# Performance work log

Measured on AMD Instinct MI355X. Metric: run time of the kernel, lower is better.

The kernel has to match this reference:

```python
import jax, jax.numpy as jnp
import numpy as np

B, T, C = 2, 2048, 1024
H = 16
D = C // H  # head_dim = 64
SCALE = D ** -0.5


def setup_inputs() -> dict:
    key = jax.random.key(0)
    ks = jax.random.split(key, 5)
    x = jax.random.normal(ks[0], (B, T, C), dtype=jnp.float32)
    # causal mask: -inf above diagonal, 0 elsewhere (module checks mask == -inf)
    neg_inf = jnp.float32(-jnp.inf)
    causal = jnp.where(jnp.tril(jnp.ones((T, T), dtype=bool)), 0.0, neg_inf)
    mask = causal[None, None, :, :].astype(jnp.float32)  # [1,1,T,T]
    # xavier_normal for [C, C] linear weights: std = sqrt(2/(C+C))
    std = float(np.sqrt(2.0 / (C + C)))
    wq = jax.random.normal(ks[1], (C, C), dtype=jnp.float32) * std
    wk = jax.random.normal(ks[2], (C, C), dtype=jnp.float32) * std
    wv = jax.random.normal(ks[3], (C, C), dtype=jnp.float32) * std
    wo = jax.random.normal(ks[4], (C, C), dtype=jnp.float32) * std
    return {"x": x, "mask": mask, "wq": wq, "wk": wk, "wv": wv, "wo": wo}


def reference(x, mask, wq, wk, wv, wo):
    # torch nn.Linear: y = x @ W.T
    q = jnp.einsum('btc,oc->bto', x, wq).reshape(B, T, H, D).transpose(0, 2, 1, 3)
    k = jnp.einsum('btc,oc->bto', x, wk).reshape(B, T, H, D).transpose(0, 2, 1, 3)
    v = jnp.einsum('btc,oc->bto', x, wv).reshape(B, T, H, D).transpose(0, 2, 1, 3)
    scores = jnp.einsum('bhqd,bhkd->bhqk', q, k) * SCALE  # [B,H,T,T]
    scores = jnp.where(mask == -jnp.inf, -jnp.inf, scores)
    attn = jax.nn.softmax(scores, axis=-1)
    out = jnp.einsum('bhqk,bhkd->bhqd', attn, v)  # [B,H,T,D]
    out = out.transpose(0, 2, 1, 3).reshape(B, T, C)
    return jnp.einsum('btc,oc->bto', out, wo)
```

## Files before the change

kernel.cpp:

```cpp
#include <hip/hip_runtime.h>
#include <hip/hip_bf16.h>


typedef __bf16 bf16_t;
typedef __bf16 bf16x8 __attribute__((ext_vector_type(8)));
typedef __bf16 bf16x4 __attribute__((ext_vector_type(4)));
typedef float  f32x4  __attribute__((ext_vector_type(4)));

__device__ __forceinline__ void gload_lds16(const bf16_t* g, bf16_t* l) {
  __builtin_amdgcn_global_load_lds((__attribute__((address_space(1))) void*)g,
                                   (__attribute__((address_space(3))) void*)l, 16, 0, 0);
}

__global__ __launch_bounds__(256) void cvt_f32_bf16(const float* __restrict__ in,
                                                    bf16_t* __restrict__ out, int n4) {
  int i = blockIdx.x * 256 + threadIdx.x;
  if (i >= n4) return;
  float4 v = reinterpret_cast<const float4*>(in)[i];
  bf16x4 o;
  o[0] = (bf16_t)v.x; o[1] = (bf16_t)v.y; o[2] = (bf16_t)v.z; o[3] = (bf16_t)v.w;
  reinterpret_cast<bf16x4*>(out)[i] = o;
}

__global__ __launch_bounds__(256) void cvt_w4(const float* __restrict__ i0, const float* __restrict__ i1,
                                              const float* __restrict__ i2, const float* __restrict__ i3,
                                              bf16_t* __restrict__ o0, bf16_t* __restrict__ o1,
                                              bf16_t* __restrict__ o2, bf16_t* __restrict__ o3) {
  int which = blockIdx.y;
  const float* in = (which == 0) ? i0 : (which == 1) ? i1 : (which == 2) ? i2 : i3;
  bf16_t* out     = (which == 0) ? o0 : (which == 1) ? o1 : (which == 2) ? o2 : o3;
  int i = blockIdx.x * 256 + threadIdx.x;
  float4 v = reinterpret_cast<const float4*>(in)[i];
  bf16x4 o;
  o[0] = (bf16_t)v.x; o[1] = (bf16_t)v.y; o[2] = (bf16_t)v.z; o[3] = (bf16_t)v.w;
  reinterpret_cast<bf16x4*>(out)[i] = o;
}

#define TM 128
#define TN 128
#define TK 64

__global__ __launch_bounds__(256) void gemm_bt(
    const bf16_t* __restrict__ A,
    const bf16_t* __restrict__ W0, const bf16_t* __restrict__ W1, const bf16_t* __restrict__ W2,
    bf16_t* __restrict__ O0, bf16_t* __restrict__ O1, bf16_t* __restrict__ O2,
    float* __restrict__ OF, int kind)
{
  __shared__ alignas(16) bf16_t As[TM * TK];
  __shared__ alignas(16) bf16_t Bs[TN * TK];
  const int K = 1024;
  const int t = threadIdx.x;
  const int lane = t & 63;
  const int w = t >> 6;
  const int wr = w >> 1, wc = w & 1;
  const int lo = lane & 15, hi = lane >> 4;
  const int m0 = blockIdx.x * TM, n0 = blockIdx.y * TN;

  int mode;
  const bf16_t* Bw;
  bf16_t* outb = nullptr;
  if (kind == 1) { mode = 3; Bw = W0; }
  else {
    mode = blockIdx.z;
    Bw   = (mode == 0) ? W0 : (mode == 1) ? W1 : W2;
    outb = (mode == 0) ? O0 : (mode == 1) ? O1 : O2;
  }

  f32x4 acc[4][4] = {};
  const int srow = t >> 3;
  const int sch  = t & 7;

  for (int k0 = 0; k0 < K; k0 += TK) {
#pragma unroll
    for (int r = 0; r < 4; ++r) {
      int row = r * 32 + srow;
      gload_lds16(A  + (size_t)(m0 + row) * K + k0 + sch * 8, &As[row * TK + sch * 8]);
      gload_lds16(Bw + (size_t)(n0 + row) * K + k0 + sch * 8, &Bs[row * TK + sch * 8]);
    }
    __syncthreads();
#pragma unroll
    for (int ks = 0; ks < 2; ++ks) {
      bf16x8 af[4], bfr[4];
#pragma unroll
      for (int i = 0; i < 4; ++i) {
        af[i]  = *reinterpret_cast<const bf16x8*>(&As[(wr * 64 + i * 16 + lo) * TK + ks * 32 + hi * 8]);
        bfr[i] = *reinterpret_cast<const bf16x8*>(&Bs[(wc * 64 + i * 16 + lo) * TK + ks * 32 + hi * 8]);
      }
#pragma unroll
      for (int i = 0; i < 4; ++i)
#pragma unroll
        for (int j = 0; j < 4; ++j)
          acc[i][j] = __builtin_amdgcn_mfma_f32_16x16x32_bf16(af[i], bfr[j], acc[i][j], 0, 0, 0);
    }
    __syncthreads();
  }

#pragma unroll
  for (int i = 0; i < 4; ++i)
#pragma unroll
    for (int j = 0; j < 4; ++j)
#pragma unroll
      for (int r = 0; r < 4; ++r) {
        int m = m0 + wr * 64 + i * 16 + hi * 4 + r;
        int n = n0 + wc * 64 + j * 16 + lo;
        float v = acc[i][j][r];
        if (mode == 3) {
          OF[(size_t)m * 1024 + n] = v;
        } else {
          int b = m >> 11, tq = m & 2047;
          int h = n >> 6,  d  = n & 63;
          if (mode == 0) v *= 0.18033688011f;
          size_t addr = (mode == 2)
              ? ((size_t)(b * 16 + h) * 64 + d) * 2048 + tq
              : ((size_t)(b * 16 + h) * 2048 + tq) * 64 + d;
          outb[addr] = (bf16_t)v;
        }
      }
}

#define SLAB 8832

__global__ __launch_bounds__(256) void attn_fwd(
    const bf16_t* __restrict__ Q,
    const bf16_t* __restrict__ Km,
    const bf16_t* __restrict__ Vt,
    bf16_t* __restrict__ att)
{
  __shared__ alignas(16) char smem[4 * SLAB];
  const int t = threadIdx.x, lane = t & 63, w = t >> 6;
  const int lo = lane & 15, hi = lane >> 4;
  const int blk = blockIdx.x;
  const int item = (blk & 7) * 128 + (blk >> 3);
  const int bh = item >> 5;
  const int pr = item & 31;
  const bf16_t* Qb = Q  + (size_t)bh * 2048 * 64;
  const bf16_t* Kb = Km + (size_t)bh * 2048 * 64;
  const bf16_t* Vb = Vt + (size_t)bh * 64 * 2048;
  bf16_t* Pw   = (bf16_t*)(smem + w * SLAB);
  float*  accW = (float*)(smem + w * SLAB);
  float*  lW   = (float*)(smem + w * SLAB + 8704);
  const int b = bh >> 4, h = bh & 15;

  auto run_tile = [&](int q0) {
    bf16x8 qf[2][2];
#pragma unroll
    for (int mi = 0; mi < 2; ++mi)
#pragma unroll
      for (int ks = 0; ks < 2; ++ks)
        qf[mi][ks] = *reinterpret_cast<const bf16x8*>(
            &Qb[(size_t)(q0 + mi * 16 + lo) * 64 + ks * 32 + hi * 8]);

    f32x4 acc[2][4] = {};
    float lp[2][4] = {};
    const int kend = q0 + 32;
    for (int kb = w * 64; kb < kend; kb += 256) {
      f32x4 s[2][4] = {};
#pragma unroll
      for (int ks = 0; ks < 2; ++ks) {
        bf16x8 kf[4];
#pragma unroll
        for (int ni = 0; ni < 4; ++ni)
          kf[ni] = *reinterpret_cast<const bf16x8*>(
              &Kb[(size_t)(kb + ni * 16 + lo) * 64 + ks * 32 + hi * 8]);
#pragma unroll
        for (int mi = 0; mi < 2; ++mi)
#pragma unroll
          for (int ni = 0; ni < 4; ++ni)
            s[mi][ni] = __builtin_amdgcn_mfma_f32_16x16x32_bf16(qf[mi][ks], kf[ni], s[mi][ni], 0, 0, 0);
      }
      bf16x8 vf[2][4];
#pragma unroll
      for (int ks2 = 0; ks2 < 2; ++ks2)
#pragma unroll
        for (int di = 0; di < 4; ++di)
          vf[ks2][di] = *reinterpret_cast<const bf16x8*>(
              &Vb[(size_t)(di * 16 + lo) * 2048 + kb + ks2 * 32 + hi * 8]);
      if (kb + 63 >= q0) {
#pragma unroll
        for (int mi = 0; mi < 2; ++mi)
#pragma unroll
          for (int ni = 0; ni < 4; ++ni)
#pragma unroll
            for (int r = 0; r < 4; ++r) {
              int row = q0 + mi * 16 + hi * 4 + r;
              int col = kb + ni * 16 + lo;
              if (col > row) s[mi][ni][r] = -__builtin_inff();
            }
      }
#pragma unroll
      for (int mi = 0; mi < 2; ++mi)
#pragma unroll
        for (int ni = 0; ni < 4; ++ni)
#pragma unroll
          for (int r = 0; r < 4; ++r) {
            float p = exp2f(s[mi][ni][r]);
            lp[mi][r] += p;
            Pw[(mi * 16 + hi * 4 + r) * 72 + ni * 16 + lo] = (bf16_t)p;
          }
#pragma unroll
      for (int ks2 = 0; ks2 < 2; ++ks2) {
        bf16x8 pa[2];
#pragma unroll
        for (int mi = 0; mi < 2; ++mi)
          pa[mi] = *reinterpret_cast<const bf16x8*>(&Pw[(mi * 16 + lo) * 72 + ks2 * 32 + hi * 8]);
#pragma unroll
        for (int mi = 0; mi < 2; ++mi)
#pragma unroll
          for (int di = 0; di < 4; ++di)
            acc[mi][di] = __builtin_amdgcn_mfma_f32_16x16x32_bf16(pa[mi], vf[ks2][di], acc[mi][di], 0, 0, 0);
      }
    }

    float lrow[2][4];
#pragma unroll
    for (int mi = 0; mi < 2; ++mi)
#pragma unroll
      for (int r = 0; r < 4; ++r) {
        float v = lp[mi][r];
        v += __shfl_xor(v, 1);
        v += __shfl_xor(v, 2);
        v += __shfl_xor(v, 4);
        v += __shfl_xor(v, 8);
        lrow[mi][r] = v;
      }

#pragma unroll
    for (int mi = 0; mi < 2; ++mi)
#pragma unroll
      for (int r = 0; r < 4; ++r) {
        int row = mi * 16 + hi * 4 + r;
#pragma unroll
        for (int di = 0; di < 4; ++di)
          accW[row * 68 + di * 16 + lo] = acc[mi][di][r];
        if (lo == 0) lW[row] = lrow[mi][r];
      }
    __syncthreads();

    {
      const int row = t >> 3, c0 = (t & 7) * 8;
      float lsum = 0.f, o[8] = {};
#pragma unroll
      for (int w2 = 0; w2 < 4; ++w2) {
        lsum += ((const float*)(smem + w2 * SLAB + 8704))[row];
        const float* a2 = (const float*)(smem + w2 * SLAB) + row * 68 + c0;
#pragma unroll
        for (int j = 0; j < 8; ++j) o[j] += a2[j];
      }
      float inv = 1.f / lsum;
      bf16x8 ov;
#pragma unroll
      for (int j = 0; j < 8; ++j) ov[j] = (bf16_t)(o[j] * inv);
      *reinterpret_cast<bf16x8*>(&att[((size_t)(b * 2048 + q0 + row)) * 1024 + h * 64 + c0]) = ov;
    }
    __syncthreads();
  };

  run_tile((63 - pr) * 32);
  run_tile(pr * 32);
}

extern "C" void kernel_launch(void* const* d_in, const int* in_sizes, int n_in,
                              void* d_out, int out_size, void* d_ws, size_t ws_size,
                              hipStream_t stream) {
  (void)in_sizes; (void)n_in; (void)out_size; (void)ws_size;
  const float* x  = (const float*)d_in[0];
  const float* wq = (const float*)d_in[2];
  const float* wk = (const float*)d_in[3];
  const float* wv = (const float*)d_in[4];
  const float* wo = (const float*)d_in[5];
  float* out = (float*)d_out;

  char* ws = (char*)d_ws;
  const size_t SZ_X = (size_t)4096 * 1024 * 2;
  const size_t SZ_W = (size_t)1024 * 1024 * 2;
  bf16_t* xb  = (bf16_t*)(ws);
  bf16_t* wqb = (bf16_t*)(ws + SZ_X);
  bf16_t* wkb = (bf16_t*)(ws + SZ_X + 1 * SZ_W);
  bf16_t* wvb = (bf16_t*)(ws + SZ_X + 2 * SZ_W);
  bf16_t* wob = (bf16_t*)(ws + SZ_X + 3 * SZ_W);
  bf16_t* qw  = (bf16_t*)(ws + 1 * SZ_X + 4 * SZ_W);
  bf16_t* kw  = (bf16_t*)(ws + 2 * SZ_X + 4 * SZ_W);
  bf16_t* vtw = (bf16_t*)(ws + 3 * SZ_X + 4 * SZ_W);
  bf16_t* att = xb;

  cvt_f32_bf16<<<4096, 256, 0, stream>>>(x, xb, 4096 * 1024 / 4);
  cvt_w4<<<dim3(1024, 4), 256, 0, stream>>>(wq, wk, wv, wo, wqb, wkb, wvb, wob);

  gemm_bt<<<dim3(32, 8, 3), 256, 0, stream>>>(xb, wqb, wkb, wvb, qw, kw, vtw, nullptr, 0);
  attn_fwd<<<1024, 256, 0, stream>>>(qw, kw, vtw, att);
  gemm_bt<<<dim3(32, 8, 1), 256, 0, stream>>>(att, wob, nullptr, nullptr,
                                              nullptr, nullptr, nullptr, out, 1);
}
```

Measured before the change: 172.0 us.

## Compute transposed scores and shuffle P into MFMA operands instead of LDS

Computes S^T (K as A operand, Q as B) so each lane holds consecutive key values for one query. The probabilities are packed to bf16 pairs and moved into the PV MFMA A-operand layout with cross-lane shuffles, which removes the LDS write/read round trip for P. The row-sum reduction shrinks to two shuffles. The change also drops the block-index swizzle and adds an occupancy hint of 4 blocks per SM in launch_bounds, which could alter cache locality and register allocation.

New measurement: 193.6 us. 1.13x slower.

```diff
diff --git a/kernel.cpp b/kernel.cpp
--- a/kernel.cpp
+++ b/kernel.cpp
@@ -5,11 +5,18 @@
 typedef __bf16 bf16_t;
 typedef __bf16 bf16x8 __attribute__((ext_vector_type(8)));
 typedef __bf16 bf16x4 __attribute__((ext_vector_type(4)));
+typedef __bf16 bf16x2 __attribute__((ext_vector_type(2)));
 typedef float  f32x4  __attribute__((ext_vector_type(4)));
+typedef unsigned u32x4 __attribute__((ext_vector_type(4)));
 
 __device__ __forceinline__ void gload_lds16(const bf16_t* g, bf16_t* l) {
   __builtin_amdgcn_global_load_lds((__attribute__((address_space(1))) void*)g,
                                    (__attribute__((address_space(3))) void*)l, 16, 0, 0);
+}
+
+__device__ __forceinline__ unsigned pack_bf16(float a, float b) {
+  bf16x2 v; v[0] = (bf16_t)a; v[1] = (bf16_t)b;
+  return __builtin_bit_cast(unsigned, v);
 }
 
 __global__ __launch_bounds__(256) void cvt_f32_bf16(const float* __restrict__ in,
@@ -120,7 +127,7 @@
 
 #define SLAB 8832
 
-__global__ __launch_bounds__(256) void attn_fwd(
+__global__ __launch_bounds__(256, 4) void attn_fwd(
     const bf16_t* __restrict__ Q,
     const bf16_t* __restrict__ Km,
     const bf16_t* __restrict__ Vt,
@@ -128,112 +135,123 @@
 {
   __shared__ alignas(16) char smem[4 * SLAB];
   const int t = threadIdx.x, lane = t & 63, w = t >> 6;
-  const int lo = lane & 15, hi = lane >> 4;
-  const int blk = blockIdx.x;
-  const int item = (blk & 7) * 128 + (blk >> 3);
+  const int lo = lane & 15, h = lane >> 4;
+  const int item = blockIdx.x;
   const int bh = item >> 5;
   const int pr = item & 31;
   const bf16_t* Qb = Q  + (size_t)bh * 2048 * 64;
   const bf16_t* Kb = Km + (size_t)bh * 2048 * 64;
   const bf16_t* Vb = Vt + (size_t)bh * 64 * 2048;
-  bf16_t* Pw   = (bf16_t*)(smem + w * SLAB);
-  float*  accW = (float*)(smem + w * SLAB);
-  float*  lW   = (float*)(smem + w * SLAB + 8704);
-  const int b = bh >> 4, h = bh & 15;
+  float* accW = (float*)(smem + w * SLAB);
+  float* lW   = (float*)(smem + w * SLAB + 8704);
+  const int b = bh >> 4, hd = bh & 15;
+  const int src1 = lo + 32 * (h & 1);
+  const int src2 = src1 + 16;
+  const bool hsel = (h >> 1) != 0;
 
   auto run_tile = [&](int q0) {
     bf16x8 qf[2][2];
 #pragma unroll
-    for (int mi = 0; mi < 2; ++mi)
+    for (int qt = 0; qt < 2; ++qt)
 #pragma unroll
       for (int ks = 0; ks < 2; ++ks)
-        qf[mi][ks] = *reinterpret_cast<const bf16x8*>(
-            &Qb[(size_t)(q0 + mi * 16 + lo) * 64 + ks * 32 + hi * 8]);
+        qf[qt][ks] = *reinterpret_cast<const bf16x8*>(
+            &Qb[(size_t)(q0 + qt * 16 + lo) * 64 + ks * 32 + h * 8]);
 
     f32x4 acc[2][4] = {};
-    float lp[2][4] = {};
+    float lp[2] = {};
     const int kend = q0 + 32;
     for (int kb = w * 64; kb < kend; kb += 256) {
-      f32x4 s[2][4] = {};
+      f32x4 s_t[4][2] = {};
 #pragma unroll
       for (int ks = 0; ks < 2; ++ks) {
         bf16x8 kf[4];
 #pragma unroll
-        for (int ni = 0; ni < 4; ++ni)
-          kf[ni] = *reinterpret_cast<const bf16x8*>(
-              &Kb[(size_t)(kb + ni * 16 + lo) * 64 + ks * 32 + hi * 8]);
-#pragma unroll
-        for (int mi = 0; mi < 2; ++mi)
-#pragma unroll
-          for (int ni = 0; ni < 4; ++ni)
-            s[mi][ni] = __builtin_amdgcn_mfma_f32_16x16x32_bf16(qf[mi][ks], kf[ni], s[mi][ni], 0, 0, 0);
+        for (int kt = 0; kt < 4; ++kt)
+          kf[kt] = *reinterpret_cast<const bf16x8*>(
+              &Kb[(size_t)(kb + kt * 16 + lo) * 64 + ks * 32 + h * 8]);
+#pragma unroll
+        for (int kt = 0; kt < 4; ++kt)
+#pragma unroll
+          for (int qt = 0; qt < 2; ++qt)
+            s_t[kt][qt] = __builtin_amdgcn_mfma_f32_16x16x32_bf16(kf[kt], qf[qt][ks], s_t[kt][qt], 0, 0, 0);
       }
       bf16x8 vf[2][4];
 #pragma unroll
-      for (int ks2 = 0; ks2 < 2; ++ks2)
-#pragma unroll
-        for (int di = 0; di < 4; ++di)
-          vf[ks2][di] = *reinterpret_cast<const bf16x8*>(
-              &Vb[(size_t)(di * 16 + lo) * 2048 + kb + ks2 * 32 + hi * 8]);
+      for (int kh = 0; kh < 2; ++kh)
+#pragma unroll
+        for (int dt = 0; dt < 4; ++dt)
+          vf[kh][dt] = *reinterpret_cast<const bf16x8*>(
+              &Vb[(size_t)(dt * 16 + lo) * 2048 + kb + kh * 32 + h * 8]);
       if (kb + 63 >= q0) {
 #pragma unroll
-        for (int mi = 0; mi < 2; ++mi)
-#pragma unroll
-          for (int ni = 0; ni < 4; ++ni)
+        for (int kt = 0; kt < 4; ++kt)
+#pragma unroll
+          for (int qt = 0; qt < 2; ++qt)
 #pragma unroll
             for (int r = 0; r < 4; ++r) {
-              int row = q0 + mi * 16 + hi * 4 + r;
-              int col = kb + ni * 16 + lo;
-              if (col > row) s[mi][ni][r] = -__builtin_inff();
+              int kg = kb + kt * 16 + h * 4 + r;
+              int qg = q0 + qt * 16 + lo;
+              if (kg > qg) s_t[kt][qt][r] = -__builtin_inff();
             }
       }
-#pragma unroll
-      for (int mi = 0; mi < 2; ++mi)
-#pragma unroll
-        for (int ni = 0; ni < 4; ++ni)
-#pragma unroll
-          for (int r = 0; r < 4; ++r) {
-            float p = exp2f(s[mi][ni][r]);
-            lp[mi][r] += p;
-            Pw[(mi * 16 + hi * 4 + r) * 72 + ni * 16 + lo] = (bf16_t)p;
-          }
-#pragma unroll
-      for (int ks2 = 0; ks2 < 2; ++ks2) {
-        bf16x8 pa[2];
-#pragma unroll
-        for (int mi = 0; mi < 2; ++mi)
-          pa[mi] = *reinterpret_cast<const bf16x8*>(&Pw[(mi * 16 + lo) * 72 + ks2 * 32 + hi * 8]);
-#pragma unroll
-        for (int mi = 0; mi < 2; ++mi)
-#pragma unroll
-          for (int di = 0; di < 4; ++di)
-            acc[mi][di] = __builtin_amdgcn_mfma_f32_16x16x32_bf16(pa[mi], vf[ks2][di], acc[mi][di], 0, 0, 0);
-      }
-    }
-
-    float lrow[2][4];
-#pragma unroll
-    for (int mi = 0; mi < 2; ++mi)
+      unsigned uP[2][4][2];
+#pragma unroll
+      for (int qt = 0; qt < 2; ++qt)
+#pragma unroll
+        for (int kt = 0; kt < 4; ++kt) {
+          float p0 = exp2f(s_t[kt][qt][0]);
+          float p1 = exp2f(s_t[kt][qt][1]);
+          float p2 = exp2f(s_t[kt][qt][2]);
+          float p3 = exp2f(s_t[kt][qt][3]);
+          lp[qt] += (p0 + p1) + (p2 + p3);
+          uP[qt][kt][0] = pack_bf16(p0, p1);
+          uP[qt][kt][1] = pack_bf16(p2, p3);
+        }
+#pragma unroll
+      for (int kh = 0; kh < 2; ++kh)
+#pragma unroll
+        for (int qt = 0; qt < 2; ++qt) {
+          unsigned a0x = __shfl((int)uP[qt][2 * kh][0], src1);
+          unsigned a0y = __shfl((int)uP[qt][2 * kh + 1][0], src1);
+          unsigned a1x = __shfl((int)uP[qt][2 * kh][1], src1);
+          unsigned a1y = __shfl((int)uP[qt][2 * kh + 1][1], src1);
+          unsigned a2x = __shfl((int)uP[qt][2 * kh][0], src2);
+          unsigned a2y = __shfl((int)uP[qt][2 * kh + 1][0], src2);
+          unsigned a3x = __shfl((int)uP[qt][2 * kh][1], src2);
+          unsigned a3y = __shfl((int)uP[qt][2 * kh + 1][1], src2);
+          u32x4 au;
+          au[0] = hsel ? a0y : a0x;
+          au[1] = hsel ? a1y : a1x;
+          au[2] = hsel ? a2y : a2x;
+          au[3] = hsel ? a3y : a3x;
+          bf16x8 pa = __builtin_bit_cast(bf16x8, au);
+#pragma unroll
+          for (int dt = 0; dt < 4; ++dt)
+            acc[qt][dt] = __builtin_amdgcn_mfma_f32_16x16x32_bf16(pa, vf[kh][dt], acc[qt][dt], 0, 0, 0);
+        }
+    }
+
+    float lrow[2];
+#pragma unroll
+    for (int qt = 0; qt < 2; ++qt) {
+      float v = lp[qt];
+      v += __shfl_xor(v, 16);
+      v += __shfl_xor(v, 32);
+      lrow[qt] = v;
+    }
+
+#pragma unroll
+    for (int qt = 0; qt < 2; ++qt) {
 #pragma unroll
       for (int r = 0; r < 4; ++r) {
-        float v = lp[mi][r];
-        v += __shfl_xor(v, 1);
-        v += __shfl_xor(v, 2);
-        v += __shfl_xor(v, 4);
-        v += __shfl_xor(v, 8);
-        lrow[mi][r] = v;
-      }
-
-#pragma unroll
-    for (int mi = 0; mi < 2; ++mi)
-#pragma unroll
-      for (int r = 0; r < 4; ++r) {
-        int row = mi * 16 + hi * 4 + r;
-#pragma unroll
-        for (int di = 0; di < 4; ++di)
-          accW[row * 68 + di * 16 + lo] = acc[mi][di][r];
-        if (lo == 0) lW[row] = lrow[mi][r];
-      }
+        int row = qt * 16 + h * 4 + r;
+#pragma unroll
+        for (int dt = 0; dt < 4; ++dt)
+          accW[row * 68 + dt * 16 + lo] = acc[qt][dt][r];
+      }
+      if (h == 0) lW[qt * 16 + lo] = lrow[qt];
+    }
     __syncthreads();
 
     {
@@ -250,7 +268,7 @@
       bf16x8 ov;
 #pragma unroll
       for (int j = 0; j < 8; ++j) ov[j] = (bf16_t)(o[j] * inv);
-      *reinterpret_cast<bf16x8*>(&att[((size_t)(b * 2048 + q0 + row)) * 1024 + h * 64 + c0]) = ov;
+      *reinterpret_cast<bf16x8*>(&att[((size_t)(b * 2048 + q0 + row)) * 1024 + hd * 64 + c0]) = ov;
     }
     __syncthreads();
   };
```
